# Performance work log

Hardware: AMD Instinct MI355X
Metric: run time of the kernel (lower is better)

Reference implementation:

```python
import jax, jax.numpy as jnp
import numpy as np

HIDDEN = 256
KSQ = 9  # 3x3 kernel


def _unfold3(x):
    # torch F.unfold(x, 3, padding=1): (N, C*9, H, W), channel-major then (ky,kx)
    N, C, H, W = x.shape
    xp = jnp.pad(x, ((0, 0), (0, 0), (1, 1), (1, 1)))
    patches = [xp[:, :, i:i + H, j:j + W] for i in range(3) for j in range(3)]
    cols = jnp.stack(patches, axis=2)  # (N, C, 9, H, W)
    return cols.reshape(N, C * KSQ, H, W)


def setup_inputs() -> dict:
    key = jax.random.key(0)
    ks = jax.random.split(key, 8)
    N, C, H, W = 1, 3, 512, 512
    OH, OW = 1024, 1024
    pos_mat = jax.random.uniform(ks[0], (N, OH, OW, 3), dtype=jnp.float32)
    mapping_mat = jax.random.randint(ks[1], (OH, OW, 2), 0, 512, dtype=jnp.int64)
    feats = jax.random.normal(ks[2], (N, C, H, W), dtype=jnp.float32)
    depth = jax.random.normal(ks[3], (N, 1, H, W), dtype=jnp.float32)
    out_ch = 1
    K = KSQ * 3 * out_ch  # 27
    W1 = jax.random.normal(ks[4], (HIDDEN, 3), dtype=jnp.float32) * 0.05
    b1 = jnp.zeros((HIDDEN,), dtype=jnp.float32)
    W2 = jax.random.normal(ks[5], (K, HIDDEN), dtype=jnp.float32) * 0.05
    b2 = jnp.zeros((K,), dtype=jnp.float32)
    return {"pos_mat": pos_mat, "mapping_mat": mapping_mat, "feats": feats,
            "depth": depth, "W1": W1, "b1": b1, "W2": W2, "b2": b2}


def reference(pos_mat, mapping_mat, feats, depth, W1, b1, W2, b2):
    N, C, H, W = feats.shape
    _, OH, OW, _ = pos_mat.shape
    P = OH * OW
    # meta-MLP: per-pixel kernel weights (P, 27)
    h = jax.nn.leaky_relu(pos_mat.reshape(P, 3) @ W1.T + b1, negative_slope=0.01)
    local_weight = h @ W2.T + b2  # (P, K)
    # im2col + irregular gather via mapping_mat
    cols = _unfold3(feats)  # (N, C*9, H, W)
    feat = cols[:, :, mapping_mat[:, :, 0], mapping_mat[:, :, 1]]  # (N, C*9, OH, OW)
    feat = feat.reshape(N, C * KSQ, P).transpose(0, 2, 1)  # (N, P, K)
    # batched tiny matmul: per-pixel dot product
    out = jnp.einsum('npk,pk->np', feat, local_weight)
    return out.reshape(N, 1, OH, OW)
```

## Files before the change

kernel.cpp:

```cpp
#include <hip/hip_runtime.h>

#define HID 256
#define K27 27

typedef __attribute__((ext_vector_type(8))) short    bf16x8;
typedef __attribute__((ext_vector_type(4))) float    f32x4;
typedef __attribute__((ext_vector_type(4))) unsigned u32x4;

static __device__ __forceinline__ unsigned short f2bf(float f) {
    union { float f; unsigned u; } v; v.f = f;
    return (unsigned short)((v.u + 0x7FFFu + ((v.u >> 16) & 1u)) >> 16);
}
static __device__ __forceinline__ unsigned pack2bf(float lo, float hi) {
    unsigned r;
    asm("v_cvt_pk_bf16_f32 %0, %1, %2" : "=v"(r) : "v"(lo), "v"(hi));
    return r;
}
static __device__ __forceinline__ bf16x8 as_bf16x8(u32x4 u) {
    return __builtin_bit_cast(bf16x8, u);
}
static __device__ __forceinline__ bf16x8 frag1(unsigned u) {
    u32x4 t = {u, 0u, 0u, 0u};
    return __builtin_bit_cast(bf16x8, t);
}
static __device__ __forceinline__ float lk(float x) {
    return fmaxf(x, 0.01f * x);
}
#define DPP_ADD(s, ctrl) \
    s += __builtin_bit_cast(float, __builtin_amdgcn_update_dpp( \
            0, __builtin_bit_cast(int, s), ctrl, 0xF, 0xF, true))

__global__ __launch_bounds__(256, 4) void mapnet_v10(
    const float* __restrict__ pos,
    const int*   __restrict__ mapping,
    const float* __restrict__ feats,
    const float* __restrict__ W1,
    const float* __restrict__ b1,
    const float* __restrict__ W2,
    const float* __restrict__ b2,
    float* __restrict__ out)
{
    __shared__ unsigned sW1f[16][64];
    __shared__ bf16x8   sB[16][64];

    const int tid = threadIdx.x;

    for (int e = tid; e < 1024; e += 256) {
        const int jt = e >> 6, l = e & 63;
        const int gg = l >> 4, cc = l & 15;
        const int j = jt * 16 + cc;
        const float val = (gg < 3) ? W1[3 * j + gg] : b1[j];
        sW1f[jt][l] = pack2bf(val, 0.0f);
    }
    for (int e = tid; e < 1024; e += 256) {
        const int kcnt = e >> 6, l = e & 63;
        const int kc = kcnt >> 1, nt = kcnt & 1;
        const int gg = l >> 4, cc = l & 15;
        const int n = nt * 16 + cc;
        const int jbase = kc * 32 + 4 * gg;
        u32x4 bb;
        #pragma unroll
        for (int i = 0; i < 4; ++i) {
            const int jlo = jbase + 16 * (i >> 1) + 2 * (i & 1);
            float f0 = 0.f, f1 = 0.f;
            if (n < K27) { f0 = W2[n * HID + jlo]; f1 = W2[n * HID + jlo + 1]; }
            bb[i] = (unsigned)f2bf(f0) | ((unsigned)f2bf(f1) << 16);
        }
        sB[kcnt][l] = as_bf16x8(bb);
    }
    __syncthreads();

    const int lane = tid & 63, wid = tid >> 6;
    const int g = lane >> 4, col = lane & 15;

    const float b2A = b2[col];
    const float b2B = (col < K27 - 16) ? b2[16 + col] : 0.0f;
    const int kA = col;
    const int cA = kA/9, dyA = (kA%9)/3 - 1, dxA = (kA%9)%3 - 1;
    const int kB = min(16 + col, K27 - 1);
    const int cB = kB/9, dyB = (kB%9)/3 - 1, dxB = (kB%9)%3 - 1;

    const float* fbaseA = feats + cA * (512*512);
    const float* fbaseB = feats + cB * (512*512);
    const int2*  map2   = (const int2*)mapping;

    const int w = blockIdx.x * 4 + wid;

    for (int it = 0; it < 4; ++it) {
        const int tb0 = (w * 8 + it * 2) * 16, tb1 = tb0 + 16;

        const float q00 = pos[3*(tb0+col)], q01 = pos[3*(tb0+col)+1], q02 = pos[3*(tb0+col)+2];
        const float q10 = pos[3*(tb1+col)], q11 = pos[3*(tb1+col)+1], q12 = pos[3*(tb1+col)+2];
        const float v0 = (g == 0) ? q00 : (g == 1) ? q01 : (g == 2) ? q02 : 1.0f;
        const float v1 = (g == 0) ? q10 : (g == 1) ? q11 : (g == 2) ? q12 : 1.0f;
        const bf16x8 pB0 = frag1(pack2bf(v0, 0.0f));
        const bf16x8 pB1 = frag1(pack2bf(v1, 0.0f));

        float fvA[2][4], fvB[2][4];
        #pragma unroll
        for (int tt = 0; tt < 2; ++tt) {
            const int tb = tt ? tb1 : tb0;
            #pragma unroll
            for (int r = 0; r < 4; ++r) {
                const int2 mp = map2[tb + g*4 + r];
                const int my = mp.x, mx = mp.y;
                int y  = my + dyA, x  = mx + dxA;
                int yc = min(max(y,0),511), xc = min(max(x,0),511);
                float f = fbaseA[yc*512 + xc];
                fvA[tt][r] = (((unsigned)y | (unsigned)x) < 512u) ? f : 0.f;
                int y2 = my + dyB, x2 = mx + dxB;
                int yc2 = min(max(y2,0),511), xc2 = min(max(x2,0),511);
                float f2 = fbaseB[yc2*512 + xc2];
                fvB[tt][r] = (((unsigned)y2 | (unsigned)x2) < 512u) ? f2 : 0.f;
            }
        }

        f32x4 acc00 = {b2A,b2A,b2A,b2A}, acc01 = {b2B,b2B,b2B,b2B};
        f32x4 acc10 = {b2A,b2A,b2A,b2A}, acc11 = {b2B,b2B,b2B,b2B};
        const f32x4 zero = {0.f, 0.f, 0.f, 0.f};

        #pragma unroll
        for (int kc = 0; kc < 8; ++kc) {
            const bf16x8 wA0 = frag1(sW1f[2*kc    ][lane]);
            const bf16x8 wA1 = frag1(sW1f[2*kc + 1][lane]);

            const f32x4 c00 = __builtin_amdgcn_mfma_f32_16x16x32_bf16(wA0, pB0, zero, 0,0,0);
            const f32x4 c01 = __builtin_amdgcn_mfma_f32_16x16x32_bf16(wA1, pB0, zero, 0,0,0);
            const f32x4 c10 = __builtin_amdgcn_mfma_f32_16x16x32_bf16(wA0, pB1, zero, 0,0,0);
            const f32x4 c11 = __builtin_amdgcn_mfma_f32_16x16x32_bf16(wA1, pB1, zero, 0,0,0);

            u32x4 a0, a1;
            a0[0] = pack2bf(lk(c00[0]), lk(c00[1]));
            a0[1] = pack2bf(lk(c00[2]), lk(c00[3]));
            a0[2] = pack2bf(lk(c01[0]), lk(c01[1]));
            a0[3] = pack2bf(lk(c01[2]), lk(c01[3]));
            a1[0] = pack2bf(lk(c10[0]), lk(c10[1]));
            a1[1] = pack2bf(lk(c10[2]), lk(c10[3]));
            a1[2] = pack2bf(lk(c11[0]), lk(c11[1]));
            a1[3] = pack2bf(lk(c11[2]), lk(c11[3]));
            const bf16x8 av0 = as_bf16x8(a0);
            const bf16x8 av1 = as_bf16x8(a1);

            const bf16x8 bv0 = sB[kc*2    ][lane];
            const bf16x8 bv1 = sB[kc*2 + 1][lane];
            acc00 = __builtin_amdgcn_mfma_f32_16x16x32_bf16(av0, bv0, acc00, 0,0,0);
            acc01 = __builtin_amdgcn_mfma_f32_16x16x32_bf16(av0, bv1, acc01, 0,0,0);
            acc10 = __builtin_amdgcn_mfma_f32_16x16x32_bf16(av1, bv0, acc10, 0,0,0);
            acc11 = __builtin_amdgcn_mfma_f32_16x16x32_bf16(av1, bv1, acc11, 0,0,0);
        }

        #pragma unroll
        for (int tt = 0; tt < 2; ++tt) {
            const int tb = tt ? tb1 : tb0;
            const f32x4 aA = tt ? acc10 : acc00;
            const f32x4 aB = tt ? acc11 : acc01;
            #pragma unroll
            for (int r = 0; r < 4; ++r) {
                float s = aA[r] * fvA[tt][r] + aB[r] * fvB[tt][r];
                DPP_ADD(s, 0xB1);
                DPP_ADD(s, 0x4E);
                DPP_ADD(s, 0x124);
                DPP_ADD(s, 0x128);
                if (col == r) out[tb + g*4 + r] = s;
            }
        }
    }
}

extern "C" void kernel_launch(void* const* d_in, const int* in_sizes, int n_in,
                              void* d_out, int out_size, void* d_ws, size_t ws_size,
                              hipStream_t stream) {
    const float* pos     = (const float*)d_in[0];
    const int*   mapping = (const int*)d_in[1];
    const float* feats   = (const float*)d_in[2];
    const float* W1      = (const float*)d_in[4];
    const float* b1      = (const float*)d_in[5];
    const float* W2      = (const float*)d_in[6];
    const float* b2      = (const float*)d_in[7];
    float* out = (float*)d_out;

    mapnet_v10<<<2048, 256, 0, stream>>>(pos, mapping, feats, W1, b1, W2, b2, out);
}
```

Baseline: 77.97 us.

## Rewrite leaky ReLU as linear combination of value and abs via doubled MFMAs

Replaces the per-element leaky ReLU on the hidden activations with the identity lrelu(x)=0.505x+0.495|x|. The raw values and their absolute values (sign bit masked in bf16) are each fed through the second-layer MFMA, and the combination plus bias is applied once per output after accumulation. This removes the per-element fmax/mul VALU work before packing, but doubles the second-layer MFMA count and accumulator registers. The launch-bounds occupancy hint is also relaxed.

```diff
diff --git a/kernel.cpp b/kernel.cpp
--- a/kernel.cpp
+++ b/kernel.cpp
@@ -23,14 +23,11 @@
     u32x4 t = {u, 0u, 0u, 0u};
     return __builtin_bit_cast(bf16x8, t);
 }
-static __device__ __forceinline__ float lk(float x) {
-    return fmaxf(x, 0.01f * x);
-}
 #define DPP_ADD(s, ctrl) \
     s += __builtin_bit_cast(float, __builtin_amdgcn_update_dpp( \
             0, __builtin_bit_cast(int, s), ctrl, 0xF, 0xF, true))
 
-__global__ __launch_bounds__(256, 4) void mapnet_v10(
+__global__ __launch_bounds__(256) void mapnet_v15(
     const float* __restrict__ pos,
     const int*   __restrict__ mapping,
     const float* __restrict__ feats,
@@ -115,9 +112,9 @@
             }
         }
 
-        f32x4 acc00 = {b2A,b2A,b2A,b2A}, acc01 = {b2B,b2B,b2B,b2B};
-        f32x4 acc10 = {b2A,b2A,b2A,b2A}, acc11 = {b2B,b2B,b2B,b2B};
         const f32x4 zero = {0.f, 0.f, 0.f, 0.f};
+        f32x4 zc00 = zero, zc01 = zero, zc10 = zero, zc11 = zero;
+        f32x4 ac00 = zero, ac01 = zero, ac10 = zero, ac11 = zero;
 
         #pragma unroll
         for (int kc = 0; kc < 8; ++kc) {
@@ -130,33 +127,46 @@
             const f32x4 c11 = __builtin_amdgcn_mfma_f32_16x16x32_bf16(wA1, pB1, zero, 0,0,0);
 
             u32x4 a0, a1;
-            a0[0] = pack2bf(lk(c00[0]), lk(c00[1]));
-            a0[1] = pack2bf(lk(c00[2]), lk(c00[3]));
-            a0[2] = pack2bf(lk(c01[0]), lk(c01[1]));
-            a0[3] = pack2bf(lk(c01[2]), lk(c01[3]));
-            a1[0] = pack2bf(lk(c10[0]), lk(c10[1]));
-            a1[1] = pack2bf(lk(c10[2]), lk(c10[3]));
-            a1[2] = pack2bf(lk(c11[0]), lk(c11[1]));
-            a1[3] = pack2bf(lk(c11[2]), lk(c11[3]));
+            a0[0] = pack2bf(c00[0], c00[1]);
+            a0[1] = pack2bf(c00[2], c00[3]);
+            a0[2] = pack2bf(c01[0], c01[1]);
+            a0[3] = pack2bf(c01[2], c01[3]);
+            a1[0] = pack2bf(c10[0], c10[1]);
+            a1[1] = pack2bf(c10[2], c10[3]);
+            a1[2] = pack2bf(c11[0], c11[1]);
+            a1[3] = pack2bf(c11[2], c11[3]);
+            u32x4 m0, m1;
+            #pragma unroll
+            for (int i = 0; i < 4; ++i) { m0[i] = a0[i] & 0x7FFF7FFFu; m1[i] = a1[i] & 0x7FFF7FFFu; }
             const bf16x8 av0 = as_bf16x8(a0);
             const bf16x8 av1 = as_bf16x8(a1);
+            const bf16x8 am0 = as_bf16x8(m0);
+            const bf16x8 am1 = as_bf16x8(m1);
 
             const bf16x8 bv0 = sB[kc*2    ][lane];
             const bf16x8 bv1 = sB[kc*2 + 1][lane];
-            acc00 = __builtin_amdgcn_mfma_f32_16x16x32_bf16(av0, bv0, acc00, 0,0,0);
-            acc01 = __builtin_amdgcn_mfma_f32_16x16x32_bf16(av0, bv1, acc01, 0,0,0);
-            acc10 = __builtin_amdgcn_mfma_f32_16x16x32_bf16(av1, bv0, acc10, 0,0,0);
-            acc11 = __builtin_amdgcn_mfma_f32_16x16x32_bf16(av1, bv1, acc11, 0,0,0);
+            zc00 = __builtin_amdgcn_mfma_f32_16x16x32_bf16(av0, bv0, zc00, 0,0,0);
+            zc01 = __builtin_amdgcn_mfma_f32_16x16x32_bf16(av0, bv1, zc01, 0,0,0);
+            zc10 = __builtin_amdgcn_mfma_f32_16x16x32_bf16(av1, bv0, zc10, 0,0,0);
+            zc11 = __builtin_amdgcn_mfma_f32_16x16x32_bf16(av1, bv1, zc11, 0,0,0);
+            ac00 = __builtin_amdgcn_mfma_f32_16x16x32_bf16(am0, bv0, ac00, 0,0,0);
+            ac01 = __builtin_amdgcn_mfma_f32_16x16x32_bf16(am0, bv1, ac01, 0,0,0);
+            ac10 = __builtin_amdgcn_mfma_f32_16x16x32_bf16(am1, bv0, ac10, 0,0,0);
+            ac11 = __builtin_amdgcn_mfma_f32_16x16x32_bf16(am1, bv1, ac11, 0,0,0);
         }
 
         #pragma unroll
         for (int tt = 0; tt < 2; ++tt) {
             const int tb = tt ? tb1 : tb0;
-            const f32x4 aA = tt ? acc10 : acc00;
-            const f32x4 aB = tt ? acc11 : acc01;
+            const f32x4 zA = tt ? zc10 : zc00;
+            const f32x4 zB = tt ? zc11 : zc01;
+            const f32x4 aA = tt ? ac10 : ac00;
+            const f32x4 aB = tt ? ac11 : ac01;
             #pragma unroll
             for (int r = 0; r < 4; ++r) {
-                float s = aA[r] * fvA[tt][r] + aB[r] * fvB[tt][r];
+                const float lwA = fmaf(0.505f, zA[r], fmaf(0.495f, aA[r], b2A));
+                const float lwB = fmaf(0.505f, zB[r], fmaf(0.495f, aB[r], b2B));
+                float s = fmaf(lwB, fvB[tt][r], lwA * fvA[tt][r]);
                 DPP_ADD(s, 0xB1);
                 DPP_ADD(s, 0x4E);
                 DPP_ADD(s, 0x124);
@@ -179,5 +189,5 @@
     const float* b2      = (const float*)d_in[7];
     float* out = (float*)d_out;
 
-    mapnet_v10<<<2048, 256, 0, stream>>>(pos, mapping, feats, W1, b1, W2, b2, out);
+    mapnet_v15<<<2048, 256, 0, stream>>>(pos, mapping, feats, W1, b1, W2, b2, out);
 }
```

Result: slower. 93.20 us (+19.5%).
